# Kernel optimization log

Measured on AMD Instinct MI355X. Metric: run time of the kernel, lower is better.

Reference implementation:

```python
import jax, jax.numpy as jnp
import numpy as np

DOWNSCALE = 2

def setup_inputs() -> dict:
    key = jax.random.key(0)
    k1, k2, k3 = jax.random.split(key, 3)
    B, C, H, W = 8, 128, 256, 256
    Cr = C // 4
    fm = jax.random.normal(k1, (B, C, H, W), dtype=jnp.float32)
    # torch Linear weight is [out,in]; store transposed [in,out] for x @ W
    Wq = jax.random.normal(k2, (C, Cr), dtype=jnp.float32) * (1.0 / np.sqrt(C))
    Wk = jax.random.normal(k3, (C, Cr), dtype=jnp.float32) * (1.0 / np.sqrt(C))
    return {"fm": fm, "Wq": Wq, "Wk": Wk}

def reference(fm, Wq, Wk):
    d = DOWNSCALE
    B, C, H, W = fm.shape
    nH, nW = H // d, W // d
    # [B,C,H,W] -> [B,nH,nW,d*d,C] windows
    x = fm.reshape(B, C, nH, d, nW, d)
    x = jnp.transpose(x, (0, 2, 4, 3, 5, 1)).reshape(B, nH, nW, d * d, C)
    # mean query over window tokens
    q = jnp.mean(x, axis=-2)                      # [B,nH,nW,C]
    q = (q @ Wq) * (Wq.shape[-1] ** -0.5)         # [B,nH,nW,Cr]
    k = x @ Wk                                    # [B,nH,nW,d*d,Cr]
    qk = jnp.einsum('bhwr,bhwtr->bhwt', q, k)     # [B,nH,nW,d*d]
    attn = jax.nn.softmax(qk, axis=-1)
    out = jnp.einsum('bhwt,bhwtc->bhwc', attn, x) # [B,nH,nW,C]
    return jnp.transpose(out, (0, 3, 1, 2))       # [B,C,nH,nW]
```

## Files before the change

### kernel.cpp

```cpp
#include <hip/hip_runtime.h>

#define BB   8
#define CCH  128
#define HH   256
#define WW   256
#define NHH  128
#define NWW  128

#define WPB  16
#define TPB  128
#define TS   68
#define QS   20

__global__ void compute_m_kernel(const float* __restrict__ Wq,
                                 const float* __restrict__ Wk,
                                 float* __restrict__ M) {
    int idx = blockIdx.x * blockDim.x + threadIdx.x;
    int cp = idx >> 7;
    int c  = idx & 127;
    float s = 0.f;
#pragma unroll
    for (int r = 0; r < 32; ++r)
        s += Wq[cp * 32 + r] * Wk[c * 32 + r];
    M[idx] = s * 0.17677669529663687f;
}

__global__ __launch_bounds__(TPB)
void attn_ds3(const float* __restrict__ fm, const float* __restrict__ M,
              float* __restrict__ out) {
    __shared__ float tile[CCH][TS];
    __shared__ float qg[CCH][QS];
    __shared__ float4 attn4[WPB];

    const int wseg = blockIdx.x;
    const int nh   = blockIdx.y;
    const int b    = blockIdx.z;
    const int t    = threadIdx.x;
    const int l    = t & 63;
    const int wv   = t >> 6;

    const int w0   = wseg * 32;
    const int row0 = nh * 2;

    const float* fmb = fm + ((size_t)(b * CCH) * HH + row0) * WW + w0;
#pragma unroll
    for (int k = 0; k < 16; ++k) {
        int q  = k * TPB + t;
        int c  = q >> 4;
        int rj = (q & 15) << 2;
        int r  = rj >> 5;
        int j  = rj & 31;
        const float4 v = *reinterpret_cast<const float4*>(
            fmb + ((size_t)c * HH + r) * WW + j);
        *reinterpret_cast<float4*>(&tile[c][rj]) = v;
    }
    __syncthreads();

    float qmA[8], qmB[8];
    {
        const int j0 = wv * 16;
        float p0[16], p1[16];
#pragma unroll
        for (int q = 0; q < 4; ++q) {
            *reinterpret_cast<float4*>(&p0[q * 4]) =
                *reinterpret_cast<const float4*>(&tile[l][j0 + q * 4]);
            *reinterpret_cast<float4*>(&p1[q * 4]) =
                *reinterpret_cast<const float4*>(&tile[l][32 + j0 + q * 4]);
        }
#pragma unroll
        for (int w = 0; w < 8; ++w)
            qmA[w] = 0.25f * (p0[2*w] + p0[2*w+1] + p1[2*w] + p1[2*w+1]);
#pragma unroll
        for (int q = 0; q < 4; ++q) {
            *reinterpret_cast<float4*>(&p0[q * 4]) =
                *reinterpret_cast<const float4*>(&tile[l + 64][j0 + q * 4]);
            *reinterpret_cast<float4*>(&p1[q * 4]) =
                *reinterpret_cast<const float4*>(&tile[l + 64][32 + j0 + q * 4]);
        }
#pragma unroll
        for (int w = 0; w < 8; ++w)
            qmB[w] = 0.25f * (p0[2*w] + p0[2*w+1] + p1[2*w] + p1[2*w+1]);
    }

    {
        float acc0[8], acc1[8];
#pragma unroll
        for (int w = 0; w < 8; ++w) { acc0[w] = 0.f; acc1[w] = 0.f; }

        const float* Mp = M + 2 * l;
#pragma unroll 4
        for (int cp = 0; cp < 64; ++cp) {
            const float2 m2 = *reinterpret_cast<const float2*>(Mp + (size_t)cp * 128);
#pragma unroll
            for (int w = 0; w < 8; ++w) {
                float qv = __int_as_float(
                    __builtin_amdgcn_readlane(__float_as_int(qmA[w]), cp));
                acc0[w] += m2.x * qv;
                acc1[w] += m2.y * qv;
            }
        }
#pragma unroll 4
        for (int cp = 0; cp < 64; ++cp) {
            const float2 m2 =
                *reinterpret_cast<const float2*>(Mp + (size_t)(cp + 64) * 128);
#pragma unroll
            for (int w = 0; w < 8; ++w) {
                float qv = __int_as_float(
                    __builtin_amdgcn_readlane(__float_as_int(qmB[w]), cp));
                acc0[w] += m2.x * qv;
                acc1[w] += m2.y * qv;
            }
        }
        *reinterpret_cast<float4*>(&qg[2*l][wv*8])     = make_float4(acc0[0], acc0[1], acc0[2], acc0[3]);
        *reinterpret_cast<float4*>(&qg[2*l][wv*8+4])   = make_float4(acc0[4], acc0[5], acc0[6], acc0[7]);
        *reinterpret_cast<float4*>(&qg[2*l+1][wv*8])   = make_float4(acc1[0], acc1[1], acc1[2], acc1[3]);
        *reinterpret_cast<float4*>(&qg[2*l+1][wv*8+4]) = make_float4(acc1[4], acc1[5], acc1[6], acc1[7]);
    }
    __syncthreads();

    {
        const int w    = t >> 3;
        const int tsub = t & 7;
        float qk0 = 0.f, qk1 = 0.f, qk2 = 0.f, qk3 = 0.f;
#pragma unroll
        for (int i = 0; i < 16; ++i) {
            int c = i * 8 + tsub;
            float g = qg[c][w];
            const float2 x0 = *reinterpret_cast<const float2*>(&tile[c][2 * w]);
            const float2 x1 = *reinterpret_cast<const float2*>(&tile[c][32 + 2 * w]);
            qk0 += g * x0.x; qk1 += g * x0.y;
            qk2 += g * x1.x; qk3 += g * x1.y;
        }
#pragma unroll
        for (int off = 1; off < 8; off <<= 1) {
            qk0 += __shfl_xor(qk0, off);
            qk1 += __shfl_xor(qk1, off);
            qk2 += __shfl_xor(qk2, off);
            qk3 += __shfl_xor(qk3, off);
        }
        float mx = fmaxf(fmaxf(qk0, qk1), fmaxf(qk2, qk3));
        float e0 = __expf(qk0 - mx);
        float e1 = __expf(qk1 - mx);
        float e2 = __expf(qk2 - mx);
        float e3 = __expf(qk3 - mx);
        float inv = 1.0f / (e0 + e1 + e2 + e3);
        if (tsub == 0)
            attn4[w] = make_float4(e0 * inv, e1 * inv, e2 * inv, e3 * inv);
    }
    __syncthreads();

    {
        const int jw = t & 15;
        const int cg = t >> 4;
        const float4 a = attn4[jw];
#pragma unroll
        for (int i = 0; i < 16; ++i) {
            int c = cg * 16 + i;
            const float2 x0 = *reinterpret_cast<const float2*>(&tile[c][2 * jw]);
            const float2 x1 = *reinterpret_cast<const float2*>(&tile[c][32 + 2 * jw]);
            out[(((size_t)(b * CCH + c)) * NHH + nh) * NWW + wseg * 16 + jw] =
                a.x * x0.x + a.y * x0.y + a.z * x1.x + a.w * x1.y;
        }
    }
}

extern "C" void kernel_launch(void* const* d_in, const int* in_sizes, int n_in,
                              void* d_out, int out_size, void* d_ws, size_t ws_size,
                              hipStream_t stream) {
    const float* fm = (const float*)d_in[0];
    const float* Wq = (const float*)d_in[1];
    const float* Wk = (const float*)d_in[2];
    float* outp = (float*)d_out;
    float* Mws  = (float*)d_ws;

    compute_m_kernel<<<dim3(64), dim3(256), 0, stream>>>(Wq, Wk, Mws);

    dim3 grid(NWW / WPB, NHH, BB);
    attn_ds3<<<grid, dim3(TPB), 0, stream>>>(fm, Mws, outp);
}
```

Measured before the change: 479.8 us.

## Compute query projection with split-bf16 MFMA and token-interleaved tile layout

Replaces the readlane-based scalar FMA loop for the 16x128x128 query-times-M product with bf16 MFMA instructions, using a hi/lo bf16 split (three MFMAs per product) to keep close to fp32 accuracy. The shared tile is reorganised so the four tokens of each 2x2 window sit contiguously, which allows float4 reads in the mean, logit and output stages. The block grows to 256 threads. This trades extra conversion work and more MFMA issues for removing the serial readlane chain; the kernel is mostly memory-bound, so the gain depends on how much of the time that compute was taking.

```diff
diff --git a/kernel.cpp b/kernel.cpp
--- a/kernel.cpp
+++ b/kernel.cpp
@@ -8,28 +8,50 @@
 #define NWW  128
 
 #define WPB  16
-#define TPB  128
-#define TS   68
-#define QS   20
-
-__global__ void compute_m_kernel(const float* __restrict__ Wq,
-                                 const float* __restrict__ Wk,
-                                 float* __restrict__ M) {
+#define TPB  256
+#define TS   72
+#define QMS  132
+
+typedef __attribute__((ext_vector_type(8))) __bf16 bf16x8;
+typedef __attribute__((ext_vector_type(4))) float f32x4;
+
+union U16x8 { ushort s[8]; int4 i4; bf16x8 v; };
+
+__device__ __forceinline__ ushort f32_to_bf16_rne(float x) {
+    unsigned u = __float_as_uint(x);
+    unsigned r = (u + 0x7FFFu + ((u >> 16) & 1u)) >> 16;
+    return (ushort)r;
+}
+__device__ __forceinline__ float bf16_to_f32(ushort h) {
+    return __uint_as_float(((unsigned)h) << 16);
+}
+
+__global__ void compute_mt_kernel(const float* __restrict__ Wq,
+                                  const float* __restrict__ Wk,
+                                  ushort* __restrict__ MT_hi,
+                                  ushort* __restrict__ MT_lo) {
     int idx = blockIdx.x * blockDim.x + threadIdx.x;
-    int cp = idx >> 7;
-    int c  = idx & 127;
+    int c  = idx >> 7;
+    int cp = idx & 127;
     float s = 0.f;
 #pragma unroll
     for (int r = 0; r < 32; ++r)
         s += Wq[cp * 32 + r] * Wk[c * 32 + r];
-    M[idx] = s * 0.17677669529663687f;
+    s *= 0.17677669529663687f;
+    ushort hi = f32_to_bf16_rne(s);
+    float  rem = s - bf16_to_f32(hi);
+    ushort lo = f32_to_bf16_rne(rem);
+    MT_hi[c * 128 + cp] = hi;
+    MT_lo[c * 128 + cp] = lo;
 }
 
 __global__ __launch_bounds__(TPB)
-void attn_ds3(const float* __restrict__ fm, const float* __restrict__ M,
+void attn_ds5(const float* __restrict__ fm,
+              const ushort* __restrict__ MT_hi,
+              const ushort* __restrict__ MT_lo,
               float* __restrict__ out) {
     __shared__ float tile[CCH][TS];
-    __shared__ float qg[CCH][QS];
+    __shared__ float qmW[WPB][QMS];
     __shared__ float4 attn4[WPB];
 
     const int wseg = blockIdx.x;
@@ -39,100 +61,100 @@
     const int l    = t & 63;
     const int wv   = t >> 6;
 
-    const int w0   = wseg * 32;
-    const int row0 = nh * 2;
-
-    const float* fmb = fm + ((size_t)(b * CCH) * HH + row0) * WW + w0;
-#pragma unroll
-    for (int k = 0; k < 16; ++k) {
-        int q  = k * TPB + t;
-        int c  = q >> 4;
-        int rj = (q & 15) << 2;
-        int r  = rj >> 5;
-        int j  = rj & 31;
-        const float4 v = *reinterpret_cast<const float4*>(
-            fmb + ((size_t)c * HH + r) * WW + j);
-        *reinterpret_cast<float4*>(&tile[c][rj]) = v;
-    }
-    __syncthreads();
-
-    float qmA[8], qmB[8];
-    {
-        const int j0 = wv * 16;
-        float p0[16], p1[16];
-#pragma unroll
-        for (int q = 0; q < 4; ++q) {
-            *reinterpret_cast<float4*>(&p0[q * 4]) =
-                *reinterpret_cast<const float4*>(&tile[l][j0 + q * 4]);
-            *reinterpret_cast<float4*>(&p1[q * 4]) =
-                *reinterpret_cast<const float4*>(&tile[l][32 + j0 + q * 4]);
-        }
-#pragma unroll
-        for (int w = 0; w < 8; ++w)
-            qmA[w] = 0.25f * (p0[2*w] + p0[2*w+1] + p1[2*w] + p1[2*w+1]);
-#pragma unroll
-        for (int q = 0; q < 4; ++q) {
-            *reinterpret_cast<float4*>(&p0[q * 4]) =
-                *reinterpret_cast<const float4*>(&tile[l + 64][j0 + q * 4]);
-            *reinterpret_cast<float4*>(&p1[q * 4]) =
-                *reinterpret_cast<const float4*>(&tile[l + 64][32 + j0 + q * 4]);
-        }
-#pragma unroll
-        for (int w = 0; w < 8; ++w)
-            qmB[w] = 0.25f * (p0[2*w] + p0[2*w+1] + p1[2*w] + p1[2*w+1]);
-    }
-
-    {
-        float acc0[8], acc1[8];
-#pragma unroll
-        for (int w = 0; w < 8; ++w) { acc0[w] = 0.f; acc1[w] = 0.f; }
-
-        const float* Mp = M + 2 * l;
-#pragma unroll 4
-        for (int cp = 0; cp < 64; ++cp) {
-            const float2 m2 = *reinterpret_cast<const float2*>(Mp + (size_t)cp * 128);
-#pragma unroll
-            for (int w = 0; w < 8; ++w) {
-                float qv = __int_as_float(
-                    __builtin_amdgcn_readlane(__float_as_int(qmA[w]), cp));
-                acc0[w] += m2.x * qv;
-                acc1[w] += m2.y * qv;
+    {
+        const float* fmb = fm + ((size_t)(b * CCH) * HH + nh * 2) * WW + wseg * 32;
+#pragma unroll
+        for (int k = 0; k < 8; ++k) {
+            int q  = k * TPB + t;
+            int c  = q >> 4;
+            int f  = q & 15;
+            int r  = f >> 3;
+            int j4 = (f & 7) << 2;
+            const float4 v = *reinterpret_cast<const float4*>(
+                fm + 0 * 0 + (size_t)0 + (fmb - fm) + ((size_t)c * HH + r) * WW + j4);
+            float vv[4] = {v.x, v.y, v.z, v.w};
+#pragma unroll
+            for (int i = 0; i < 4; ++i) {
+                int jj  = j4 + i;
+                int w   = jj >> 1;
+                int tok = (r << 1) | (jj & 1);
+                tile[c][(w << 2) | tok] = vv[i];
             }
         }
-#pragma unroll 4
-        for (int cp = 0; cp < 64; ++cp) {
-            const float2 m2 =
-                *reinterpret_cast<const float2*>(Mp + (size_t)(cp + 64) * 128);
-#pragma unroll
-            for (int w = 0; w < 8; ++w) {
-                float qv = __int_as_float(
-                    __builtin_amdgcn_readlane(__float_as_int(qmB[w]), cp));
-                acc0[w] += m2.x * qv;
-                acc1[w] += m2.y * qv;
+    }
+    __syncthreads();
+
+    {
+        const int c     = t & 127;
+        const int whalf = t >> 7;
+#pragma unroll
+        for (int k = 0; k < 8; ++k) {
+            int w = whalf * 8 + ((k + (c & 7)) & 7);
+            const float4 x4 = *reinterpret_cast<const float4*>(&tile[c][w << 2]);
+            qmW[w][c] = 0.25f * (x4.x + x4.y + x4.z + x4.w);
+        }
+    }
+    __syncthreads();
+
+    {
+        const int wrow = l & 15;
+        const int lq   = l >> 4;
+        f32x4 acc0 = {0.f, 0.f, 0.f, 0.f};
+        f32x4 acc1 = {0.f, 0.f, 0.f, 0.f};
+        const int ct0 = 2 * wv, ct1 = 2 * wv + 1;
+
+#pragma unroll
+        for (int kk = 0; kk < 4; ++kk) {
+            const float* ap = &qmW[wrow][kk * 32 + lq * 8];
+            const float4 a0 = *reinterpret_cast<const float4*>(ap);
+            const float4 a1 = *reinterpret_cast<const float4*>(ap + 4);
+            float af[8] = {a0.x, a0.y, a0.z, a0.w, a1.x, a1.y, a1.z, a1.w};
+            U16x8 Ah, Al;
+#pragma unroll
+            for (int j = 0; j < 8; ++j) {
+                ushort hi = f32_to_bf16_rne(af[j]);
+                Ah.s[j] = hi;
+                Al.s[j] = f32_to_bf16_rne(af[j] - bf16_to_f32(hi));
             }
-        }
-        *reinterpret_cast<float4*>(&qg[2*l][wv*8])     = make_float4(acc0[0], acc0[1], acc0[2], acc0[3]);
-        *reinterpret_cast<float4*>(&qg[2*l][wv*8+4])   = make_float4(acc0[4], acc0[5], acc0[6], acc0[7]);
-        *reinterpret_cast<float4*>(&qg[2*l+1][wv*8])   = make_float4(acc1[0], acc1[1], acc1[2], acc1[3]);
-        *reinterpret_cast<float4*>(&qg[2*l+1][wv*8+4]) = make_float4(acc1[4], acc1[5], acc1[6], acc1[7]);
-    }
-    __syncthreads();
-
-    {
-        const int w    = t >> 3;
-        const int tsub = t & 7;
+            const size_t bo0 = (size_t)(ct0 * 16 + wrow) * 128 + kk * 32 + lq * 8;
+            const size_t bo1 = (size_t)(ct1 * 16 + wrow) * 128 + kk * 32 + lq * 8;
+            U16x8 Bh0, Bl0, Bh1, Bl1;
+            Bh0.i4 = *reinterpret_cast<const int4*>(MT_hi + bo0);
+            Bl0.i4 = *reinterpret_cast<const int4*>(MT_lo + bo0);
+            Bh1.i4 = *reinterpret_cast<const int4*>(MT_hi + bo1);
+            Bl1.i4 = *reinterpret_cast<const int4*>(MT_lo + bo1);
+
+            acc0 = __builtin_amdgcn_mfma_f32_16x16x32_bf16(Ah.v, Bh0.v, acc0, 0, 0, 0);
+            acc0 = __builtin_amdgcn_mfma_f32_16x16x32_bf16(Ah.v, Bl0.v, acc0, 0, 0, 0);
+            acc0 = __builtin_amdgcn_mfma_f32_16x16x32_bf16(Al.v, Bh0.v, acc0, 0, 0, 0);
+            acc1 = __builtin_amdgcn_mfma_f32_16x16x32_bf16(Ah.v, Bh1.v, acc1, 0, 0, 0);
+            acc1 = __builtin_amdgcn_mfma_f32_16x16x32_bf16(Ah.v, Bl1.v, acc1, 0, 0, 0);
+            acc1 = __builtin_amdgcn_mfma_f32_16x16x32_bf16(Al.v, Bh1.v, acc1, 0, 0, 0);
+        }
+        __syncthreads();
+
+#pragma unroll
+        for (int r = 0; r < 4; ++r) {
+            qmW[lq * 4 + r][ct0 * 16 + wrow] = acc0[r];
+            qmW[lq * 4 + r][ct1 * 16 + wrow] = acc1[r];
+        }
+    }
+    __syncthreads();
+
+    {
+        const int w    = t >> 4;
+        const int tsub = t & 15;
         float qk0 = 0.f, qk1 = 0.f, qk2 = 0.f, qk3 = 0.f;
 #pragma unroll
-        for (int i = 0; i < 16; ++i) {
-            int c = i * 8 + tsub;
-            float g = qg[c][w];
-            const float2 x0 = *reinterpret_cast<const float2*>(&tile[c][2 * w]);
-            const float2 x1 = *reinterpret_cast<const float2*>(&tile[c][32 + 2 * w]);
-            qk0 += g * x0.x; qk1 += g * x0.y;
-            qk2 += g * x1.x; qk3 += g * x1.y;
-        }
-#pragma unroll
-        for (int off = 1; off < 8; off <<= 1) {
+        for (int i = 0; i < 8; ++i) {
+            int c = i * 16 + tsub;
+            float g = qmW[w][c];
+            const float4 x4 = *reinterpret_cast<const float4*>(&tile[c][w << 2]);
+            qk0 += g * x4.x; qk1 += g * x4.y;
+            qk2 += g * x4.z; qk3 += g * x4.w;
+        }
+#pragma unroll
+        for (int off = 1; off < 16; off <<= 1) {
             qk0 += __shfl_xor(qk0, off);
             qk1 += __shfl_xor(qk1, off);
             qk2 += __shfl_xor(qk2, off);
@@ -154,12 +176,11 @@
         const int cg = t >> 4;
         const float4 a = attn4[jw];
 #pragma unroll
-        for (int i = 0; i < 16; ++i) {
-            int c = cg * 16 + i;
-            const float2 x0 = *reinterpret_cast<const float2*>(&tile[c][2 * jw]);
-            const float2 x1 = *reinterpret_cast<const float2*>(&tile[c][32 + 2 * jw]);
-            out[(((size_t)(b * CCH + c)) * NHH + nh) * NWW + wseg * 16 + jw] =
-                a.x * x0.x + a.y * x0.y + a.z * x1.x + a.w * x1.y;
+        for (int i = 0; i < 8; ++i) {
+            int c = cg * 8 + i;
+            const float4 x4 = *reinterpret_cast<const float4*>(&tile[c][jw << 2]);
+            float o = a.x * x4.x + a.y * x4.y + a.z * x4.z + a.w * x4.w;
+            out[(((size_t)(b * CCH + c)) * NHH + nh) * NWW + wseg * 16 + jw] = o;
         }
     }
 }
@@ -171,10 +192,11 @@
     const float* Wq = (const float*)d_in[1];
     const float* Wk = (const float*)d_in[2];
     float* outp = (float*)d_out;
-    float* Mws  = (float*)d_ws;
-
-    compute_m_kernel<<<dim3(64), dim3(256), 0, stream>>>(Wq, Wk, Mws);
+    ushort* MT_hi = (ushort*)d_ws;
+    ushort* MT_lo = (ushort*)d_ws + 128 * 128;
+
+    compute_mt_kernel<<<dim3(64), dim3(256), 0, stream>>>(Wq, Wk, MT_hi, MT_lo);
 
     dim3 grid(NWW / WPB, NHH, BB);
-    attn_ds3<<<grid, dim3(TPB), 0, stream>>>(fm, Mws, outp);
-}
+    attn_ds5<<<grid, dim3(TPB), 0, stream>>>(fm, MT_hi, MT_lo, outp);
+}
```

After: 417.9 us. 12.9% less time.
